# Performance work log

Hardware: AMD Instinct MI355X
Metric: run time of the kernel (lower is better)

## Reference

```python
import jax, jax.numpy as jnp
import numpy as np

B, C, LX, LY, H = 8, 128, 4096, 1024, 4
DH = C // H


def setup_inputs() -> dict:
    key = jax.random.key(0)
    ks = jax.random.split(key, 12)
    s = 0.05
    return {
        "x": jax.random.normal(ks[0], (B, C, LX), jnp.float32),
        "y": jax.random.normal(ks[1], (B, C, LY), jnp.float32),
        # nn.MultiheadAttention combined in-projection [3C, C] and bias [3C]
        "in_proj_w": jax.random.normal(ks[2], (3 * C, C), jnp.float32) * s,
        "in_proj_b": jax.random.normal(ks[3], (3 * C,), jnp.float32) * s,
        # local_att: Conv1d(C,32,1) then Conv1d(32,1,1); kernel_size=1 -> stored as matrices
        "conv1_w": jax.random.normal(ks[4], (32, C), jnp.float32) * s,
        "conv1_b": jax.random.normal(ks[5], (32,), jnp.float32) * s,
        "conv2_w": jax.random.normal(ks[6], (1, 32), jnp.float32) * s,
        "conv2_b": jax.random.normal(ks[7], (1,), jnp.float32) * s,
        # gate_mlp: Linear(2, 1)
        "gate_w": jax.random.normal(ks[8], (1, 2), jnp.float32) * s,
        "gate_b": jax.random.normal(ks[9], (1,), jnp.float32) * s,
    }


def reference(x, y, in_proj_w, in_proj_b, conv1_w, conv1_b, conv2_w, conv2_b, gate_w, gate_b):
    # x: [B,C,Lx] (query side), y: [B,C,Ly] (key/value side)
    wq, wk = in_proj_w[:C], in_proj_w[C:2 * C]
    bq, bk = in_proj_b[:C], in_proj_b[C:2 * C]

    xt = jnp.swapaxes(x, 1, 2)  # [B,Lx,C]
    yt = jnp.swapaxes(y, 1, 2)  # [B,Ly,C]

    q = (xt @ wq.T + bq).reshape(B, LX, H, DH)
    k = (yt @ wk.T + bk).reshape(B, LY, H, DH)

    scores = jnp.einsum('bqhd,bkhd->bhqk', q, k) / jnp.sqrt(jnp.float32(DH))  # [B,H,Lx,Ly]
    attn = jax.nn.softmax(scores, axis=-1)
    # torch MHA returns head-averaged weights (average_attn_weights=True)
    cross_weights = attn.mean(axis=1)            # [B,Lx,Ly]
    cross_scores = cross_weights.max(axis=-1)    # [B,Lx]
    # (attn_output / V / out_proj are unused downstream in the original forward)

    # local conv scoring (1x1 convs == channel matmuls)
    h = jax.nn.relu(jnp.einsum('oc,bcl->bol', conv1_w, x) + conv1_b[None, :, None])
    local_scores = jax.nn.sigmoid(jnp.einsum('po,bol->bpl', conv2_w, h) + conv2_b[None, :, None])[:, 0, :]  # [B,Lx]

    gating = jnp.stack((cross_scores, local_scores), axis=-1)  # [B,Lx,2]
    alpha = jax.nn.sigmoid(gating @ gate_w.T + gate_b)[..., 0]  # [B,Lx]
    return alpha * cross_scores + (1.0 - alpha) * local_scores
```

## Files before the change

kernel.cpp:

```cpp
#include <hip/hip_runtime.h>
#include <hip/hip_bf16.h>

#define BB  8
#define CC  128
#define LXX 4096
#define LYY 1024
#define HH  4
#define DHH 32

typedef __attribute__((ext_vector_type(8))) short bf16x8;
typedef __attribute__((ext_vector_type(4))) float f32x4;

static __device__ __forceinline__ unsigned short f2bf(float f) {
    __hip_bfloat16 h = __float2bfloat16(f);
    return *reinterpret_cast<unsigned short*>(&h);
}

static __device__ __forceinline__ bf16x8 pack8(const float* f) {
    bf16x8 r;
#pragma unroll
    for (int i = 0; i < 8; ++i) {
        __hip_bfloat16 h = __float2bfloat16(f[i]);
        r[i] = *reinterpret_cast<short*>(&h);
    }
    return r;
}

__global__ __launch_bounds__(256) void proj_all_kernel(
    const float* __restrict__ x, const float* __restrict__ y,
    const float* __restrict__ ipw, const float* __restrict__ ipb,
    const float* __restrict__ c1w, const float* __restrict__ c1b,
    const float* __restrict__ c2w, const float* __restrict__ c2b,
    unsigned short* __restrict__ Qb, unsigned short* __restrict__ Kb,
    float* __restrict__ localS, float qscale)
{
    int tid  = threadIdx.x;
    int wv   = tid >> 6;
    int lane = tid & 63;
    int n16  = lane & 15;
    int quad = lane >> 4;

    int blk = blockIdx.x;
    bool isX = (blk < 512);
    const float* src; const float* wrow; const float* bias;
    unsigned short* dst; int L, bi, l0; float scale;
    if (isX) {
        bi = blk >> 6; l0 = (blk & 63) * 64;
        src = x + (size_t)bi * CC * LXX; L = LXX;
        wrow = ipw; bias = ipb; dst = Qb; scale = qscale;
    } else {
        int b2 = blk - 512;
        bi = b2 >> 4; l0 = (b2 & 15) * 64;
        src = y + (size_t)bi * CC * LYY; L = LYY;
        wrow = ipw + CC * CC; bias = ipb + CC; dst = Kb; scale = 1.0f;
    }
    int lw = l0 + wv * 16;
    int myl = lw + n16;

    bf16x8 bfr[4];
#pragma unroll
    for (int kk = 0; kk < 4; ++kk) {
        float t[8];
        const float* p = src + (size_t)(kk * 32 + quad * 8) * L + myl;
#pragma unroll
        for (int j = 0; j < 8; ++j) t[j] = p[(size_t)j * L];
        bfr[kk] = pack8(t);
    }

    const f32x4 fzero = {0.f, 0.f, 0.f, 0.f};

#pragma unroll 1
    for (int m = 0; m < 8; ++m) {
        int mc = m * 16;
        f32x4 acc = fzero;
#pragma unroll
        for (int kk = 0; kk < 4; ++kk) {
            const float* wp = wrow + (size_t)(mc + n16) * CC + kk * 32 + quad * 8;
            float t[8];
            *(float4*)(t) = *(const float4*)(wp);
            *(float4*)(t + 4) = *(const float4*)(wp + 4);
            bf16x8 afr = pack8(t);
            acc = __builtin_amdgcn_mfma_f32_16x16x32_bf16(afr, bfr[kk], acc, 0, 0, 0);
        }
        int h = mc >> 5, d0 = (mc & 31) + quad * 4;
        ushort4 u;
        float4 bq = *(const float4*)(bias + mc + quad * 4);
        u.x = f2bf((acc[0] + bq.x) * scale);
        u.y = f2bf((acc[1] + bq.y) * scale);
        u.z = f2bf((acc[2] + bq.z) * scale);
        u.w = f2bf((acc[3] + bq.w) * scale);
        *(ushort4*)(dst + (((size_t)(bi * HH + h) * L) + myl) * DHH + d0) = u;
    }

    if (isX) {
        float p = 0.f;
#pragma unroll
        for (int m2 = 0; m2 < 2; ++m2) {
            f32x4 hacc = fzero;
#pragma unroll
            for (int kk = 0; kk < 4; ++kk) {
                const float* wp = c1w + (size_t)(m2 * 16 + n16) * CC + kk * 32 + quad * 8;
                float t[8];
                *(float4*)(t) = *(const float4*)(wp);
                *(float4*)(t + 4) = *(const float4*)(wp + 4);
                bf16x8 afr = pack8(t);
                hacc = __builtin_amdgcn_mfma_f32_16x16x32_bf16(afr, bfr[kk], hacc, 0, 0, 0);
            }
#pragma unroll
            for (int r = 0; r < 4; ++r) {
                int o = m2 * 16 + quad * 4 + r;
                p = fmaf(c2w[o], fmaxf(hacc[r] + c1b[o], 0.0f), p);
            }
        }
        p += __shfl_xor(p, 16, 64);
        p += __shfl_xor(p, 32, 64);
        if (quad == 0) {
            float s = p + c2b[0];
            localS[(size_t)bi * LXX + myl] = 1.0f / (1.0f + __expf(-s));
        }
    }
}

__global__ __launch_bounds__(256, 3) void attn_kernel(
    const unsigned short* __restrict__ Qh, const unsigned short* __restrict__ Kh,
    const float* __restrict__ localS,
    const float* __restrict__ gw, const float* __restrict__ gb,
    float* __restrict__ out)
{
    int tid = threadIdx.x;
    int wave = tid >> 6;
    int lane = tid & 63;
    int n16 = lane & 15;
    int quad = lane >> 4;
    int bi = blockIdx.y;
    int q0 = blockIdx.x * 16;
    int row = quad * 4;

    __shared__ float lbuf[HH][4][16];
    __shared__ float mbuf[4][16];

    const unsigned short* Qp = Qh + (((size_t)bi * HH) * LXX + q0 + n16) * DHH + quad * 8;
    const unsigned short* Kp = Kh + (((size_t)bi * HH) * LYY + wave * 256 + n16) * DHH + quad * 8;

    const f32x4 fzero = {0.f, 0.f, 0.f, 0.f};
    f32x4 vAcc[16];
#pragma unroll
    for (int t = 0; t < 16; ++t) vAcc[t] = fzero;

#pragma unroll 1
    for (int h = 0; h < HH; ++h) {
        bf16x8 afr = *(const bf16x8*)(Qp + (size_t)h * LXX * DHH);
        const unsigned short* Kph = Kp + (size_t)h * LYY * DHH;
        f32x4 s[16];
#pragma unroll
        for (int t = 0; t < 16; ++t) {
            bf16x8 bfr = *(const bf16x8*)(Kph + (size_t)t * 16 * DHH);
            s[t] = __builtin_amdgcn_mfma_f32_16x16x32_bf16(afr, bfr, fzero, 0, 0, 0);
        }
        float lr[4] = {0.f, 0.f, 0.f, 0.f};
#pragma unroll
        for (int t = 0; t < 16; ++t)
#pragma unroll
            for (int r = 0; r < 4; ++r) {
                float e = __builtin_amdgcn_exp2f(s[t][r]);
                s[t][r] = e;
                lr[r] += e;
            }
#pragma unroll
        for (int off = 1; off < 16; off <<= 1)
#pragma unroll
            for (int r = 0; r < 4; ++r) lr[r] += __shfl_xor(lr[r], off, 64);
        if (n16 == 0) {
#pragma unroll
            for (int r = 0; r < 4; ++r) lbuf[h][wave][row + r] = lr[r];
        }
        __syncthreads();
#pragma unroll
        for (int r = 0; r < 4; ++r) {
            float inv = 1.0f / (lbuf[h][0][row + r] + lbuf[h][1][row + r] +
                                lbuf[h][2][row + r] + lbuf[h][3][row + r]);
#pragma unroll
            for (int t = 0; t < 16; ++t) vAcc[t][r] += s[t][r] * inv;
        }
    }
    float vm[4] = {-1e30f, -1e30f, -1e30f, -1e30f};
#pragma unroll
    for (int t = 0; t < 16; ++t)
#pragma unroll
        for (int r = 0; r < 4; ++r) vm[r] = fmaxf(vm[r], vAcc[t][r]);
#pragma unroll
    for (int off = 1; off < 16; off <<= 1)
#pragma unroll
        for (int r = 0; r < 4; ++r) vm[r] = fmaxf(vm[r], __shfl_xor(vm[r], off, 64));
    if (n16 == 0) {
#pragma unroll
        for (int r = 0; r < 4; ++r) mbuf[wave][row + r] = vm[r];
    }
    __syncthreads();
    if (tid < 16) {
        float cs = 0.25f * fmaxf(fmaxf(mbuf[0][tid], mbuf[1][tid]), fmaxf(mbuf[2][tid], mbuf[3][tid]));
        float ls = localS[(size_t)bi * LXX + q0 + tid];
        float z = gw[0] * cs + gw[1] * ls + gb[0];
        float alpha = 1.0f / (1.0f + __expf(-z));
        out[(size_t)bi * LXX + q0 + tid] = alpha * cs + (1.0f - alpha) * ls;
    }
}

extern "C" void kernel_launch(void* const* d_in, const int* in_sizes, int n_in,
                              void* d_out, int out_size, void* d_ws, size_t ws_size,
                              hipStream_t stream) {
    const float* x   = (const float*)d_in[0];
    const float* y   = (const float*)d_in[1];
    const float* ipw = (const float*)d_in[2];
    const float* ipb = (const float*)d_in[3];
    const float* c1w = (const float*)d_in[4];
    const float* c1b = (const float*)d_in[5];
    const float* c2w = (const float*)d_in[6];
    const float* c2b = (const float*)d_in[7];
    const float* gw  = (const float*)d_in[8];
    const float* gb  = (const float*)d_in[9];
    float* out = (float*)d_out;

    float* localS = (float*)d_ws;
    unsigned short* Qb = (unsigned short*)(localS + 32768);
    unsigned short* Kb = Qb + (size_t)BB * HH * LXX * DHH;

    const float qscale = 0.17677669529663687f * 1.4426950408889634f;

    hipLaunchKernelGGL(proj_all_kernel, dim3(640), dim3(256), 0, stream,
                       x, y, ipw, ipb, c1w, c1b, c2w, c2b, Qb, Kb, localS, qscale);
    hipLaunchKernelGGL(attn_kernel, dim3(LXX / 16, BB), dim3(256), 0, stream,
                       Qb, Kb, localS, gw, gb, out);
}
```

Before: 154.1 us.

## Restructure attention into two-pass per-wave softmax with log-denominator folded into MFMA

Each wave now processes 32 queries over all keys and heads in two passes. The first pass accumulates softmax denominators; the second recomputes the scores with -log(den) injected as the MFMA accumulator so exp2 yields normalized probabilities directly. This removes the shared-memory exchange and block barriers and reuses each K fragment across two query tiles. In exchange it doubles the MFMA and exp work and launches far fewer blocks, which reduces occupancy.

```diff
diff --git a/kernel.cpp b/kernel.cpp
--- a/kernel.cpp
+++ b/kernel.cpp
@@ -121,7 +121,7 @@
     }
 }
 
-__global__ __launch_bounds__(256, 3) void attn_kernel(
+__global__ __launch_bounds__(256, 1) void attn_kernel(
     const unsigned short* __restrict__ Qh, const unsigned short* __restrict__ Kh,
     const float* __restrict__ localS,
     const float* __restrict__ gw, const float* __restrict__ gb,
@@ -133,76 +133,107 @@
     int n16 = lane & 15;
     int quad = lane >> 4;
     int bi = blockIdx.y;
-    int q0 = blockIdx.x * 16;
-    int row = quad * 4;
-
-    __shared__ float lbuf[HH][4][16];
-    __shared__ float mbuf[4][16];
-
-    const unsigned short* Qp = Qh + (((size_t)bi * HH) * LXX + q0 + n16) * DHH + quad * 8;
-    const unsigned short* Kp = Kh + (((size_t)bi * HH) * LYY + wave * 256 + n16) * DHH + quad * 8;
+    int q0 = blockIdx.x * 128 + wave * 32;
 
     const f32x4 fzero = {0.f, 0.f, 0.f, 0.f};
-    f32x4 vAcc[16];
-#pragma unroll
-    for (int t = 0; t < 16; ++t) vAcc[t] = fzero;
-
-#pragma unroll 1
-    for (int h = 0; h < HH; ++h) {
-        bf16x8 afr = *(const bf16x8*)(Qp + (size_t)h * LXX * DHH);
-        const unsigned short* Kph = Kp + (size_t)h * LYY * DHH;
-        f32x4 s[16];
-#pragma unroll
-        for (int t = 0; t < 16; ++t) {
-            bf16x8 bfr = *(const bf16x8*)(Kph + (size_t)t * 16 * DHH);
-            s[t] = __builtin_amdgcn_mfma_f32_16x16x32_bf16(afr, bfr, fzero, 0, 0, 0);
-        }
-        float lr[4] = {0.f, 0.f, 0.f, 0.f};
-#pragma unroll
-        for (int t = 0; t < 16; ++t)
-#pragma unroll
-            for (int r = 0; r < 4; ++r) {
-                float e = __builtin_amdgcn_exp2f(s[t][r]);
-                s[t][r] = e;
-                lr[r] += e;
-            }
-#pragma unroll
-        for (int off = 1; off < 16; off <<= 1)
-#pragma unroll
-            for (int r = 0; r < 4; ++r) lr[r] += __shfl_xor(lr[r], off, 64);
-        if (n16 == 0) {
-#pragma unroll
-            for (int r = 0; r < 4; ++r) lbuf[h][wave][row + r] = lr[r];
-        }
-        __syncthreads();
+
+    bf16x8 afr[2][4];
+#pragma unroll
+    for (int qt = 0; qt < 2; ++qt)
+#pragma unroll
+        for (int h = 0; h < HH; ++h)
+            afr[qt][h] = *(const bf16x8*)(Qh +
+                (((size_t)bi * HH + h) * LXX + q0 + qt * 16 + n16) * DHH + quad * 8);
+
+    const unsigned short* Kbase = Kh + ((size_t)bi * HH * LYY + n16) * DHH + quad * 8;
+
+    f32x4 den[2][HH];
+#pragma unroll
+    for (int qt = 0; qt < 2; ++qt)
+#pragma unroll
+        for (int h = 0; h < HH; ++h) den[qt][h] = fzero;
+
+#pragma unroll 2
+    for (int t = 0; t < 64; ++t) {
+        bf16x8 bfr[HH];
+#pragma unroll
+        for (int h = 0; h < HH; ++h)
+            bfr[h] = *(const bf16x8*)(Kbase + ((size_t)h * LYY + t * 16) * DHH);
+#pragma unroll
+        for (int h = 0; h < HH; ++h) {
+            f32x4 s0 = __builtin_amdgcn_mfma_f32_16x16x32_bf16(afr[0][h], bfr[h], fzero, 0, 0, 0);
+            f32x4 s1 = __builtin_amdgcn_mfma_f32_16x16x32_bf16(afr[1][h], bfr[h], fzero, 0, 0, 0);
+#pragma unroll
+            for (int r = 0; r < 4; ++r) {
+                den[0][h][r] += __builtin_amdgcn_exp2f(s0[r]);
+                den[1][h][r] += __builtin_amdgcn_exp2f(s1[r]);
+            }
+        }
+    }
+#pragma unroll
+    for (int off = 1; off < 16; off <<= 1)
+#pragma unroll
+        for (int qt = 0; qt < 2; ++qt)
+#pragma unroll
+            for (int h = 0; h < HH; ++h)
+#pragma unroll
+                for (int r = 0; r < 4; ++r)
+                    den[qt][h][r] += __shfl_xor(den[qt][h][r], off, 64);
+
+    f32x4 cc[2][HH];
+#pragma unroll
+    for (int qt = 0; qt < 2; ++qt)
+#pragma unroll
+        for (int h = 0; h < HH; ++h)
+#pragma unroll
+            for (int r = 0; r < 4; ++r)
+                cc[qt][h][r] = -__builtin_amdgcn_logf(den[qt][h][r]);
+
+    f32x4 vm0 = fzero, vm1 = fzero;
+#pragma unroll 2
+    for (int t = 0; t < 64; ++t) {
+        bf16x8 bfr[HH];
+#pragma unroll
+        for (int h = 0; h < HH; ++h)
+            bfr[h] = *(const bf16x8*)(Kbase + ((size_t)h * LYY + t * 16) * DHH);
+        f32x4 f0 = fzero, f1 = fzero;
+#pragma unroll
+        for (int h = 0; h < HH; ++h) {
+            f32x4 s0 = __builtin_amdgcn_mfma_f32_16x16x32_bf16(afr[0][h], bfr[h], cc[0][h], 0, 0, 0);
+            f32x4 s1 = __builtin_amdgcn_mfma_f32_16x16x32_bf16(afr[1][h], bfr[h], cc[1][h], 0, 0, 0);
+#pragma unroll
+            for (int r = 0; r < 4; ++r) {
+                f0[r] += __builtin_amdgcn_exp2f(s0[r]);
+                f1[r] += __builtin_amdgcn_exp2f(s1[r]);
+            }
+        }
 #pragma unroll
         for (int r = 0; r < 4; ++r) {
-            float inv = 1.0f / (lbuf[h][0][row + r] + lbuf[h][1][row + r] +
-                                lbuf[h][2][row + r] + lbuf[h][3][row + r]);
-#pragma unroll
-            for (int t = 0; t < 16; ++t) vAcc[t][r] += s[t][r] * inv;
-        }
-    }
-    float vm[4] = {-1e30f, -1e30f, -1e30f, -1e30f};
-#pragma unroll
-    for (int t = 0; t < 16; ++t)
-#pragma unroll
-        for (int r = 0; r < 4; ++r) vm[r] = fmaxf(vm[r], vAcc[t][r]);
+            vm0[r] = fmaxf(vm0[r], f0[r]);
+            vm1[r] = fmaxf(vm1[r], f1[r]);
+        }
+    }
 #pragma unroll
     for (int off = 1; off < 16; off <<= 1)
 #pragma unroll
-        for (int r = 0; r < 4; ++r) vm[r] = fmaxf(vm[r], __shfl_xor(vm[r], off, 64));
+        for (int r = 0; r < 4; ++r) {
+            vm0[r] = fmaxf(vm0[r], __shfl_xor(vm0[r], off, 64));
+            vm1[r] = fmaxf(vm1[r], __shfl_xor(vm1[r], off, 64));
+        }
+
     if (n16 == 0) {
-#pragma unroll
-        for (int r = 0; r < 4; ++r) mbuf[wave][row + r] = vm[r];
-    }
-    __syncthreads();
-    if (tid < 16) {
-        float cs = 0.25f * fmaxf(fmaxf(mbuf[0][tid], mbuf[1][tid]), fmaxf(mbuf[2][tid], mbuf[3][tid]));
-        float ls = localS[(size_t)bi * LXX + q0 + tid];
-        float z = gw[0] * cs + gw[1] * ls + gb[0];
-        float alpha = 1.0f / (1.0f + __expf(-z));
-        out[(size_t)bi * LXX + q0 + tid] = alpha * cs + (1.0f - alpha) * ls;
+        float g0 = gw[0], g1 = gw[1], gbv = gb[0];
+#pragma unroll
+        for (int qt = 0; qt < 2; ++qt)
+#pragma unroll
+            for (int r = 0; r < 4; ++r) {
+                int row = q0 + qt * 16 + quad * 4 + r;
+                float cs = 0.25f * (qt == 0 ? vm0[r] : vm1[r]);
+                float ls = localS[(size_t)bi * LXX + row];
+                float z = g0 * cs + g1 * ls + gbv;
+                float alpha = 1.0f / (1.0f + __expf(-z));
+                out[(size_t)bi * LXX + row] = alpha * cs + (1.0f - alpha) * ls;
+            }
     }
 }
 
@@ -229,6 +260,6 @@
 
     hipLaunchKernelGGL(proj_all_kernel, dim3(640), dim3(256), 0, stream,
                        x, y, ipw, ipb, c1w, c1b, c2w, c2b, Qb, Kb, localS, qscale);
-    hipLaunchKernelGGL(attn_kernel, dim3(LXX / 16, BB), dim3(256), 0, stream,
+    hipLaunchKernelGGL(attn_kernel, dim3(LXX / 128, BB), dim3(256), 0, stream,
                        Qb, Kb, localS, gw, gb, out);
 }
```

After: 175.5 us. 13.9% more time.
